# Kernel optimization log

Measured on AMD Instinct MI355X. Metric: run time of the kernel, lower is better.

The kernel has to match this reference:

```python
import jax, jax.numpy as jnp
import numpy as np

B, F, D, E, V1 = 16384, 26, 13, 16, 100001  # V1 = vocab + 1 (padding row 0)
H1, H2 = 128, 64
IN_DIM = F * E + D  # 429
EPS = 1e-5


def setup_inputs() -> dict:
    key = jax.random.key(0)
    ks = jax.random.split(key, 16)
    u = lambda k, shape, s=0.001: jax.random.uniform(k, shape, jnp.float32, -s, s)
    sparse_inputs = jax.random.randint(ks[0], (B, F), 0, V1, dtype=jnp.int32)
    dense_inputs = jax.random.normal(ks[1], (B, D), jnp.float32)
    emb_tables = u(ks[2], (F, V1, E)).at[:, 0, :].set(0.0)   # padding_idx=0 zeroed
    lin_tables = u(ks[3], (F, V1)).at[:, 0].set(0.0)
    lin_dense_w = u(ks[4], (D,))
    lin_dense_b = jnp.zeros((1,), jnp.float32)
    # BatchNorm (eval mode): gamma, beta, running_mean, running_var
    bn0 = (jnp.ones(IN_DIM), jnp.zeros(IN_DIM), 0.01 * jax.random.normal(ks[5], (IN_DIM,)), jnp.ones(IN_DIM))
    W1 = jax.random.normal(ks[6], (H1, IN_DIM)) * (1.0 / np.sqrt(IN_DIM))
    b1 = jnp.zeros(H1)
    bn1 = (jnp.ones(H1), jnp.zeros(H1), 0.01 * jax.random.normal(ks[7], (H1,)), jnp.ones(H1))
    W2 = jax.random.normal(ks[8], (H2, H1)) * (1.0 / np.sqrt(H1))
    b2 = jnp.zeros(H2)
    bn2 = (jnp.ones(H2), jnp.zeros(H2), 0.01 * jax.random.normal(ks[9], (H2,)), jnp.ones(H2))
    Wo = u(ks[10], (1, H2))
    bo = jnp.zeros(1)
    gbias = jnp.zeros(1)
    return dict(sparse_inputs=sparse_inputs, dense_inputs=dense_inputs,
                emb_tables=emb_tables, lin_tables=lin_tables,
                lin_dense_w=lin_dense_w, lin_dense_b=lin_dense_b,
                bn0_g=bn0[0], bn0_b=bn0[1], bn0_m=bn0[2], bn0_v=bn0[3],
                W1=W1, b1=b1, bn1_g=bn1[0], bn1_b=bn1[1], bn1_m=bn1[2], bn1_v=bn1[3],
                W2=W2, b2=b2, bn2_g=bn2[0], bn2_b=bn2[1], bn2_m=bn2[2], bn2_v=bn2[3],
                Wo=Wo, bo=bo, gbias=gbias)


def _bn(x, g, b, m, v):
    return (x - m) * jax.lax.rsqrt(v + EPS) * g + b


def reference(sparse_inputs, dense_inputs, emb_tables, lin_tables,
              lin_dense_w, lin_dense_b,
              bn0_g, bn0_b, bn0_m, bn0_v,
              W1, b1, bn1_g, bn1_b, bn1_m, bn1_v,
              W2, b2, bn2_g, bn2_b, bn2_m, bn2_v,
              Wo, bo, gbias):
    # gather per-feature embedding rows: [B, F, E] and linear terms [B, F]
    emb = jax.vmap(lambda tab, ix: tab[ix], in_axes=(0, 1), out_axes=1)(emb_tables, sparse_inputs)
    lin = jax.vmap(lambda tab, ix: tab[ix], in_axes=(0, 1), out_axes=1)(lin_tables, sparse_inputs)

    linear_sparse = jnp.sum(lin, axis=1, keepdims=True)                       # [B,1]
    linear_dense = dense_inputs @ lin_dense_w[:, None] + lin_dense_b          # [B,1]

    # FM: 0.5 * ((sum_f e)^2 - sum_f e^2), summed over embedding dim
    s = jnp.sum(emb, axis=1)
    fm = 0.5 * jnp.sum(s * s - jnp.sum(emb * emb, axis=1), axis=1, keepdims=True)  # [B,1]

    deep_in = jnp.concatenate([emb.reshape(emb.shape[0], -1), dense_inputs], axis=1)  # [B, F*E+D]
    h = _bn(deep_in, bn0_g, bn0_b, bn0_m, bn0_v)
    h = jax.nn.relu(_bn(h @ W1.T + b1, bn1_g, bn1_b, bn1_m, bn1_v))
    h = jax.nn.relu(_bn(h @ W2.T + b2, bn2_g, bn2_b, bn2_m, bn2_v))
    deep_out = h @ Wo.T + bo                                                   # [B,1]

    out = gbias + linear_sparse + linear_dense + fm + deep_out
    return out.squeeze(-1)
```

## Files before the change

### kernel.cpp

```cpp
#include <hip/hip_runtime.h>

#define BATCH  16384
#define NF     26
#define ND     13
#define NE     16
#define V1     100001
#define H1     128
#define H2     64
#define IN_DIM 429
#define KPAD   448
#define EPS    1e-5f

#define BM     32
#define NT     512
#define SD     456
#define SH     136

typedef __attribute__((ext_vector_type(8))) short short8;
typedef __attribute__((ext_vector_type(4))) float f32x4;

static __device__ __forceinline__ unsigned short f2bf(float x) {
    unsigned int u = __float_as_uint(x);
    unsigned int r = (u + 0x7FFFu + ((u >> 16) & 1u)) >> 16;
    return (unsigned short)r;
}
static __device__ __forceinline__ float bf2f(unsigned short s) {
    return __uint_as_float(((unsigned int)s) << 16);
}

__global__ __launch_bounds__(256) void prep_kernel(
    const float* __restrict__ bn0_g, const float* __restrict__ bn0_b,
    const float* __restrict__ bn0_m, const float* __restrict__ bn0_v,
    const float* __restrict__ W1,    const float* __restrict__ b1,
    const float* __restrict__ bn1_g, const float* __restrict__ bn1_b,
    const float* __restrict__ bn1_m, const float* __restrict__ bn1_v,
    const float* __restrict__ W2,    const float* __restrict__ b2,
    const float* __restrict__ bn2_g, const float* __restrict__ bn2_b,
    const float* __restrict__ bn2_m, const float* __restrict__ bn2_v,
    const float* __restrict__ bo,    const float* __restrict__ gbias,
    const float* __restrict__ ldb,
    unsigned short* __restrict__ packB1, unsigned short* __restrict__ packB2,
    float* __restrict__ ceff, float* __restrict__ c2, float* __restrict__ constv)
{
    const int blk = blockIdx.x, tid = threadIdx.x;

    if (blk < 28) {
        int t    = blk * 256 + tid;
        int nblk = t / (14 * 64);
        int rem  = t % (14 * 64);
        int ks   = rem >> 6;
        int l    = rem & 63;
        int col  = nblk * 16 + (l & 15);
        float a1 = bn1_g[col] * rsqrtf(bn1_v[col] + EPS);
        int k0   = ks * 32 + ((l >> 4) << 3);
        union { short8 v; unsigned short u[8]; } tmp;
        #pragma unroll
        for (int j = 0; j < 8; ++j) {
            int k = k0 + j;
            float v = 0.f;
            if (k < IN_DIM) {
                float a0 = bn0_g[k] * rsqrtf(bn0_v[k] + EPS);
                v = W1[col * IN_DIM + k] * a0 * a1;
            }
            tmp.u[j] = f2bf(v);
        }
        *reinterpret_cast<short8*>(packB1 + (size_t)t * 8) = tmp.v;
    } else if (blk < 32) {
        int t    = (blk - 28) * 256 + tid;
        int nblk = t >> 8;
        int rem  = t & 255;
        int ks   = rem >> 6;
        int l    = rem & 63;
        int col  = nblk * 16 + (l & 15);
        float a2 = bn2_g[col] * rsqrtf(bn2_v[col] + EPS);
        int k0   = ks * 32 + ((l >> 4) << 3);
        union { short8 v; unsigned short u[8]; } tmp;
        #pragma unroll
        for (int j = 0; j < 8; ++j) {
            int k = k0 + j;
            tmp.u[j] = f2bf(W2[col * H1 + k] * a2);
        }
        *reinterpret_cast<short8*>(packB2 + (size_t)t * 8) = tmp.v;
    } else if (blk < 40) {
        int w = tid >> 6, l = tid & 63;
        #pragma unroll
        for (int i = 0; i < 4; ++i) {
            int o = (blk - 32) * 16 + w * 4 + i;
            float sum = 0.f;
            #pragma unroll
            for (int it = 0; it < 7; ++it) {
                int k = l + it * 64;
                if (k < IN_DIM) {
                    float a0 = bn0_g[k] * rsqrtf(bn0_v[k] + EPS);
                    float u0 = bn0_b[k] - a0 * bn0_m[k];
                    sum += u0 * W1[o * IN_DIM + k];
                }
            }
            sum += __shfl_xor(sum, 32);
            sum += __shfl_xor(sum, 16);
            sum += __shfl_xor(sum, 8);
            sum += __shfl_xor(sum, 4);
            sum += __shfl_xor(sum, 2);
            sum += __shfl_xor(sum, 1);
            if (l == 0) {
                float a1 = bn1_g[o] * rsqrtf(bn1_v[o] + EPS);
                ceff[o] = a1 * (sum + b1[o] - bn1_m[o]) + bn1_b[o];
            }
        }
    } else {
        if (tid < H2) {
            float a2 = bn2_g[tid] * rsqrtf(bn2_v[tid] + EPS);
            c2[tid] = a2 * (b2[tid] - bn2_m[tid]) + bn2_b[tid];
        } else if (tid == 64) {
            constv[0] = gbias[0] + bo[0] + ldb[0];
        }
    }
}

__global__ __launch_bounds__(NT, 4) void deepfm_main(
    const int*   __restrict__ sparse, const float* __restrict__ dense,
    const float* __restrict__ emb,    const float* __restrict__ lin,
    const float* __restrict__ ldw,
    const unsigned short* __restrict__ packB1,
    const unsigned short* __restrict__ packB2,
    const float* __restrict__ ceff, const float* __restrict__ c2w,
    const float* __restrict__ Wo,   const float* __restrict__ constv,
    float* __restrict__ out)
{
    __shared__ __align__(16) unsigned short deepS[BM][SD];
    __shared__ __align__(16) unsigned short h1S[BM][SH];
    __shared__ __align__(16) int sparseS[BM * NF];
    __shared__ float accS[BM];

    const int tid = threadIdx.x;
    const int r0  = blockIdx.x * BM;

    if (tid < BM) accS[tid] = constv[0];
    {
        int z = tid;
        if (z < BM * (KPAD - IN_DIM)) {
            int row = z / (KPAD - IN_DIM), c = IN_DIM + z % (KPAD - IN_DIM);
            deepS[row][c] = 0;
        }
        z = tid + NT;
        if (z < BM * (KPAD - IN_DIM)) {
            int row = z / (KPAD - IN_DIM), c = IN_DIM + z % (KPAD - IN_DIM);
            deepS[row][c] = 0;
        }
    }
    if (tid < BM * NF / 2) {
        reinterpret_cast<int2*>(sparseS)[tid] =
            reinterpret_cast<const int2*>(sparse + (size_t)r0 * NF)[tid];
    }
    __syncthreads();

    #pragma unroll
    for (int it = 0; it < 7; ++it) {
        int q = tid + it * NT;
        if (q < BM * NF * 4) {
            int p = q >> 2, quarter = q & 3;
            int row = p / NF, f = p - row * NF;
            int idx = sparseS[p];
            const float* src = emb + ((size_t)f * V1 + (size_t)idx) * NE + quarter * 4;
            float4 v = *reinterpret_cast<const float4*>(src);
            ushort4 sv = { f2bf(v.x), f2bf(v.y), f2bf(v.z), f2bf(v.w) };
            *reinterpret_cast<ushort4*>(&deepS[row][f * NE + quarter * 4]) = sv;
            if (quarter == 0) {
                atomicAdd(&accS[row], lin[(size_t)f * V1 + (size_t)idx]);
            }
        }
    }
    if (tid < BM * ND) {
        int row = tid / ND, j = tid - row * ND;
        float v = dense[(r0 + row) * ND + j];
        deepS[row][NF * NE + j] = f2bf(v);
        atomicAdd(&accS[row], v * ldw[j]);
    }
    __syncthreads();

    {
        int row = tid >> 4, e = tid & 15;
        float s = 0.f, ss = 0.f;
        #pragma unroll
        for (int f = 0; f < NF; ++f) {
            float x = bf2f(deepS[row][f * NE + e]);
            s += x; ss += x * x;
        }
        float fmv = 0.5f * (s * s - ss);
        fmv += __shfl_xor(fmv, 1);
        fmv += __shfl_xor(fmv, 2);
        fmv += __shfl_xor(fmv, 4);
        fmv += __shfl_xor(fmv, 8);
        if (e == 0) atomicAdd(&accS[row], fmv);
    }

    const int w = tid >> 6, l = tid & 63;
    const int lr = l & 15, lq = l >> 4;

    f32x4 acc1[2] = { {0.f,0.f,0.f,0.f}, {0.f,0.f,0.f,0.f} };
    const short8* pB1 = reinterpret_cast<const short8*>(packB1);
    #pragma unroll
    for (int ks = 0; ks < KPAD / 32; ++ks) {
        short8 aF0 = *reinterpret_cast<const short8*>(&deepS[lr     ][ks * 32 + lq * 8]);
        short8 aF1 = *reinterpret_cast<const short8*>(&deepS[16 + lr][ks * 32 + lq * 8]);
        short8 bF  = pB1[((size_t)w * 14 + ks) * 64 + l];
        acc1[0] = __builtin_amdgcn_mfma_f32_16x16x32_bf16(aF0, bF, acc1[0], 0, 0, 0);
        acc1[1] = __builtin_amdgcn_mfma_f32_16x16x32_bf16(aF1, bF, acc1[1], 0, 0, 0);
    }
    {
        int col = w * 16 + lr;
        float ce = ceff[col];
        #pragma unroll
        for (int mb = 0; mb < 2; ++mb) {
            #pragma unroll
            for (int r = 0; r < 4; ++r) {
                float h = fmaxf(acc1[mb][r] + ce, 0.f);
                h1S[mb * 16 + lq * 4 + r][col] = f2bf(h);
            }
        }
    }
    __syncthreads();

    const int mblk2 = w >> 2, nb2 = w & 3;
    f32x4 acc2 = { 0.f, 0.f, 0.f, 0.f };
    const short8* pB2 = reinterpret_cast<const short8*>(packB2);
    #pragma unroll
    for (int ks = 0; ks < 4; ++ks) {
        short8 aF = *reinterpret_cast<const short8*>(&h1S[mblk2 * 16 + lr][ks * 32 + lq * 8]);
        short8 bF = pB2[((size_t)nb2 * 4 + ks) * 64 + l];
        acc2 = __builtin_amdgcn_mfma_f32_16x16x32_bf16(aF, bF, acc2, 0, 0, 0);
    }
    {
        int col = nb2 * 16 + lr;
        float cv = c2w[col], wv = Wo[col];
        float part[4];
        #pragma unroll
        for (int r = 0; r < 4; ++r)
            part[r] = fmaxf(acc2[r] + cv, 0.f) * wv;
        #pragma unroll
        for (int r = 0; r < 4; ++r) {
            part[r] += __shfl_xor(part[r], 1);
            part[r] += __shfl_xor(part[r], 2);
            part[r] += __shfl_xor(part[r], 4);
            part[r] += __shfl_xor(part[r], 8);
        }
        if (lr == 0) {
            #pragma unroll
            for (int r = 0; r < 4; ++r)
                atomicAdd(&accS[mblk2 * 16 + lq * 4 + r], part[r]);
        }
    }
    __syncthreads();

    if (tid < BM) out[r0 + tid] = accS[tid];
}

extern "C" void kernel_launch(void* const* d_in, const int* in_sizes, int n_in,
                              void* d_out, int out_size, void* d_ws, size_t ws_size,
                              hipStream_t stream) {
    const int*   sparse = (const int*)d_in[0];
    const float* dense  = (const float*)d_in[1];
    const float* emb    = (const float*)d_in[2];
    const float* lin    = (const float*)d_in[3];
    const float* ldw    = (const float*)d_in[4];
    const float* ldb    = (const float*)d_in[5];
    const float* bn0g = (const float*)d_in[6],  *bn0b = (const float*)d_in[7];
    const float* bn0m = (const float*)d_in[8],  *bn0v = (const float*)d_in[9];
    const float* W1   = (const float*)d_in[10], *b1   = (const float*)d_in[11];
    const float* bn1g = (const float*)d_in[12], *bn1b = (const float*)d_in[13];
    const float* bn1m = (const float*)d_in[14], *bn1v = (const float*)d_in[15];
    const float* W2   = (const float*)d_in[16], *b2   = (const float*)d_in[17];
    const float* bn2g = (const float*)d_in[18], *bn2b = (const float*)d_in[19];
    const float* bn2m = (const float*)d_in[20], *bn2v = (const float*)d_in[21];
    const float* Wo   = (const float*)d_in[22], *bo   = (const float*)d_in[23];
    const float* gbias = (const float*)d_in[24];

    char* ws = (char*)d_ws;
    unsigned short* packB1 = (unsigned short*)ws;
    unsigned short* packB2 = (unsigned short*)(ws + 114688);
    float* ceff   = (float*)(ws + 131072);
    float* c2     = (float*)(ws + 131584);
    float* constv = (float*)(ws + 131840);

    prep_kernel<<<41, 256, 0, stream>>>(
        bn0g, bn0b, bn0m, bn0v, W1, b1, bn1g, bn1b, bn1m, bn1v,
        W2, b2, bn2g, bn2b, bn2m, bn2v, bo, gbias, ldb,
        packB1, packB2, ceff, c2, constv);

    deepfm_main<<<BATCH / BM, NT, 0, stream>>>(
        sparse, dense, emb, lin, ldw, packB1, packB2, ceff, c2, Wo, constv,
        (float*)d_out);
}
```

Before: 272.5 us.

## Drop prologue barrier and LDS atomics, fold linear terms into FM reduction

The kernel no longer stages sparse indices into shared memory behind an initial barrier; each thread reads its index straight from global memory. The shared-memory atomicAdds for the sparse and dense linear terms are replaced by per-row scratch arrays. Those values are summed inside the existing FM shuffle reduction, and a single thread per row writes the accumulator. Launch bounds are also raised from 4 to 6 blocks per CU. Shared-memory use probably cannot reach that occupancy, so the main effect may be a tighter register cap with some risk of spills.

```diff
diff --git a/kernel.cpp b/kernel.cpp
--- a/kernel.cpp
+++ b/kernel.cpp
@@ -117,7 +117,7 @@
     }
 }
 
-__global__ __launch_bounds__(NT, 4) void deepfm_main(
+__global__ __launch_bounds__(NT, 6) void deepfm_main(
     const int*   __restrict__ sparse, const float* __restrict__ dense,
     const float* __restrict__ emb,    const float* __restrict__ lin,
     const float* __restrict__ ldw,
@@ -129,30 +129,12 @@
 {
     __shared__ __align__(16) unsigned short deepS[BM][SD];
     __shared__ __align__(16) unsigned short h1S[BM][SH];
-    __shared__ __align__(16) int sparseS[BM * NF];
+    __shared__ float linS[BM][NF];
+    __shared__ float dlinS[BM][ND];
     __shared__ float accS[BM];
 
     const int tid = threadIdx.x;
     const int r0  = blockIdx.x * BM;
-
-    if (tid < BM) accS[tid] = constv[0];
-    {
-        int z = tid;
-        if (z < BM * (KPAD - IN_DIM)) {
-            int row = z / (KPAD - IN_DIM), c = IN_DIM + z % (KPAD - IN_DIM);
-            deepS[row][c] = 0;
-        }
-        z = tid + NT;
-        if (z < BM * (KPAD - IN_DIM)) {
-            int row = z / (KPAD - IN_DIM), c = IN_DIM + z % (KPAD - IN_DIM);
-            deepS[row][c] = 0;
-        }
-    }
-    if (tid < BM * NF / 2) {
-        reinterpret_cast<int2*>(sparseS)[tid] =
-            reinterpret_cast<const int2*>(sparse + (size_t)r0 * NF)[tid];
-    }
-    __syncthreads();
 
     #pragma unroll
     for (int it = 0; it < 7; ++it) {
@@ -160,21 +142,33 @@
         if (q < BM * NF * 4) {
             int p = q >> 2, quarter = q & 3;
             int row = p / NF, f = p - row * NF;
-            int idx = sparseS[p];
+            int idx = sparse[r0 * NF + p];
             const float* src = emb + ((size_t)f * V1 + (size_t)idx) * NE + quarter * 4;
             float4 v = *reinterpret_cast<const float4*>(src);
             ushort4 sv = { f2bf(v.x), f2bf(v.y), f2bf(v.z), f2bf(v.w) };
             *reinterpret_cast<ushort4*>(&deepS[row][f * NE + quarter * 4]) = sv;
             if (quarter == 0) {
-                atomicAdd(&accS[row], lin[(size_t)f * V1 + (size_t)idx]);
-            }
+                linS[row][f] = lin[(size_t)f * V1 + (size_t)idx];
+            }
+        }
+    }
+    {
+        int z = tid;
+        if (z < BM * (KPAD - IN_DIM)) {
+            int row = z / (KPAD - IN_DIM), c = IN_DIM + z % (KPAD - IN_DIM);
+            deepS[row][c] = 0;
+        }
+        z = tid + NT;
+        if (z < BM * (KPAD - IN_DIM)) {
+            int row = z / (KPAD - IN_DIM), c = IN_DIM + z % (KPAD - IN_DIM);
+            deepS[row][c] = 0;
         }
     }
     if (tid < BM * ND) {
         int row = tid / ND, j = tid - row * ND;
         float v = dense[(r0 + row) * ND + j];
         deepS[row][NF * NE + j] = f2bf(v);
-        atomicAdd(&accS[row], v * ldw[j]);
+        dlinS[row][j] = v * ldw[j];
     }
     __syncthreads();
 
@@ -186,12 +180,15 @@
             float x = bf2f(deepS[row][f * NE + e]);
             s += x; ss += x * x;
         }
-        float fmv = 0.5f * (s * s - ss);
-        fmv += __shfl_xor(fmv, 1);
-        fmv += __shfl_xor(fmv, 2);
-        fmv += __shfl_xor(fmv, 4);
-        fmv += __shfl_xor(fmv, 8);
-        if (e == 0) atomicAdd(&accS[row], fmv);
+        float t = 0.5f * (s * s - ss);
+        t += linS[row][e];
+        if (e < NF - 16) t += linS[row][16 + e];
+        if (e < ND)      t += dlinS[row][e];
+        t += __shfl_xor(t, 1);
+        t += __shfl_xor(t, 2);
+        t += __shfl_xor(t, 4);
+        t += __shfl_xor(t, 8);
+        if (e == 0) accS[row] = constv[0] + t;
     }
 
     const int w = tid >> 6, l = tid & 63;
```

New measurement: 272.1 us. No clear change (-0.1%).
